# Kernel optimization log

Hardware: AMD Instinct MI355X
Metric: run time of the kernel (lower is better)

Reference implementation:

```python
import jax, jax.numpy as jnp
import numpy as np

DIM = 1024
H = 16
D = DIM // H
CS = 64  # chunk_size
SCALE = D ** -0.5


def setup_inputs() -> dict:
    key = jax.random.key(0)
    k1, k2, k3 = jax.random.split(key, 3)
    B, N = 4, 4096
    x = jax.random.normal(k1, (B, N, DIM), dtype=jnp.float32)
    # torch nn.Linear(dim, 3*dim, bias=False): y = x @ W.T, W:[3*dim, dim].
    # We store the transposed layout W_qkv:[dim, 3*dim] so y = x @ W_qkv.
    W_qkv = jax.random.normal(k2, (DIM, 3 * DIM), dtype=jnp.float32) * (DIM ** -0.5)
    W_out = jax.random.normal(k3, (DIM, DIM), dtype=jnp.float32) * (DIM ** -0.5)
    return {"x": x, "W_qkv": W_qkv, "W_out": W_out}


def reference(x, W_qkv, W_out):
    B, N, C = x.shape
    qkv = (x @ W_qkv).reshape(B, N, 3, H, D)
    qkv = jnp.transpose(qkv, (2, 0, 3, 1, 4))  # [3,B,H,N,D]
    q, k, v = qkv[0], qkv[1], qkv[2]
    # N chosen divisible by CS, so no padding needed (pad=0 branch).
    nc = N // CS
    q = q.reshape(B, H, nc, CS, D)
    k = k.reshape(B, H, nc, CS, D)
    v = v.reshape(B, H, nc, CS, D)
    # Local quadratic attention within each chunk, causal mask.
    attn = jnp.einsum('bhcqd,bhckd->bhcqk', q, k) * SCALE
    mask = jnp.triu(jnp.ones((CS, CS), dtype=bool), k=1)
    attn = jnp.where(mask, jnp.float32(-65000.0), attn)
    attn = jax.nn.softmax(attn, axis=-1)
    out_local = jnp.einsum('bhcqk,bhckd->bhcqd', attn, v)
    # Cross-chunk linear term (num_chunks > 1): mean-pooled K/V, exclusive cumsum.
    chunk_k = k.mean(axis=3)  # [B,H,nc,D]
    chunk_v = v.mean(axis=3)
    cum_k = jnp.cumsum(chunk_k, axis=2)
    cum_v = jnp.cumsum(chunk_v, axis=2)
    zeros = jnp.zeros((B, H, 1, D), dtype=x.dtype)
    cum_k = jnp.concatenate([zeros, cum_k[:, :, :-1]], axis=2)
    cum_v = jnp.concatenate([zeros, cum_v[:, :, :-1]], axis=2)
    cross = jax.nn.sigmoid(jnp.einsum('bhcsd,bhcd->bhcs', q, cum_k) * SCALE)
    out = out_local + cross[..., None] * cum_v[:, :, :, None, :] * 0.5
    out = out.reshape(B, H, N, D)
    out = jnp.transpose(out, (0, 2, 1, 3)).reshape(B, N, C)
    return out @ W_out
```

## Files before the change

### kernel.cpp

```cpp
#include <hip/hip_runtime.h>
#include <stdint.h>

typedef __attribute__((ext_vector_type(4))) float f32x4;
typedef __attribute__((ext_vector_type(8))) short short8;
typedef unsigned short u16;

#define NH 16
#define HD 64
#define SEQ 4096
#define BATCH 4
#define NROWS (BATCH * SEQ)
#define DIMC 1024
#define QKVC 3072
#define SCALE 0.125f

__device__ __forceinline__ u16 f2bf(float f) {
  union { float f; uint32_t u; } v; v.f = f;
  uint32_t u = v.u;
  uint32_t r = (u + 0x7fffu + ((u >> 16) & 1u)) >> 16;
  return (u16)r;
}
__device__ __forceinline__ float bf2f(u16 h) {
  union { uint32_t u; float f; } v; v.u = ((uint32_t)h) << 16;
  return v.f;
}

__global__ __launch_bounds__(256) void cvt_kernel(const float* __restrict__ in,
                                                  u16* __restrict__ out, int n4) {
  int i = blockIdx.x * 256 + threadIdx.x;
  if (i >= n4) return;
  float4 v = ((const float4*)in)[i];
  ushort4 o;
  o.x = f2bf(v.x); o.y = f2bf(v.y); o.z = f2bf(v.z); o.w = f2bf(v.w);
  ((ushort4*)out)[i] = o;
}

__global__ __launch_bounds__(256) void transpose_cvt(const float* __restrict__ in,
                                                     u16* __restrict__ out, int R, int C) {
  __shared__ float t[32][33];
  int nbx = C >> 5;
  int bx = blockIdx.x % nbx, by = blockIdx.x / nbx;
  int r0 = by << 5, c0 = bx << 5;
  int tid = threadIdx.x;
#pragma unroll
  for (int i = 0; i < 4; i++) {
    int id = i * 256 + tid; int lr = id >> 5, lc = id & 31;
    t[lr][lc] = in[(size_t)(r0 + lr) * C + (c0 + lc)];
  }
  __syncthreads();
#pragma unroll
  for (int i = 0; i < 4; i++) {
    int id = i * 256 + tid; int lr = id >> 5, lc = id & 31;
    out[(size_t)(c0 + lr) * R + (r0 + lc)] = f2bf(t[lc][lr]);
  }
}

template <int OUT_BF16, int DO_SUMS>
__global__ __launch_bounds__(512, 2) void gemm_bt(const u16* __restrict__ A,
                                                  const u16* __restrict__ Bt,
                                                  void* __restrict__ Cv,
                                                  float* __restrict__ chk,
                                                  float* __restrict__ chv,
                                                  int M, int N, int K) {
  __shared__ __align__(16) u16 lds2[2][32768];
  int nbx = N >> 8;
  int nwg = gridDim.x;
  int bid = blockIdx.x;
  int cpx = nwg >> 3;
  int swz = (bid & 7) * cpx + (bid >> 3);
  int bx = swz % nbx, by = swz / nbx;
  int tid = threadIdx.x, lane = tid & 63, wv = tid >> 6;
  int wr = wv >> 2, wc = wv & 3;
  int lr = lane & 15, g = lane >> 4;
  int rx = lr & 7;
  int rsub = lane >> 3;
  int clog = (lane & 7) ^ rsub;

  const u16* Ap = A + (size_t)(by * 256) * K;
  const u16* Bp = Bt + (size_t)(bx * 256) * K;

  f32x4 acc[8][4];
#pragma unroll
  for (int m = 0; m < 8; m++)
#pragma unroll
    for (int n = 0; n < 4; n++) acc[m][n] = (f32x4){0.f, 0.f, 0.f, 0.f};

  short8 a0[4][2], a1[4][2], b0[2][2], b1[2][2];

#define ISSUE_A(HALF, L, T) do {                                                \
    int ru_ = (HALF) * 128 + (L) * 64 + wv * 8;                                 \
    const u16* g_ = Ap + (size_t)(ru_ + rsub) * K + (T) * 64 + clog * 8;        \
    __builtin_amdgcn_global_load_lds(                                           \
        (const __attribute__((address_space(1))) uint32_t*)g_,                  \
        (__attribute__((address_space(3))) uint32_t*)&lds2[(T) & 1][ru_ * 64],  \
        16, 0, 0);                                                              \
  } while (0)

#define ISSUE_B(HALF, L, T) do {                                                \
    int ru_ = (HALF) * 128 + (L) * 64 + wv * 8;                                 \
    const u16* g_ = Bp + (size_t)(ru_ + rsub) * K + (T) * 64 + clog * 8;        \
    __builtin_amdgcn_global_load_lds(                                           \
        (const __attribute__((address_space(1))) uint32_t*)g_,                  \
        (__attribute__((address_space(3)))                                      \
             uint32_t*)&lds2[(T) & 1][16384 + ru_ * 64],                        \
        16, 0, 0);                                                              \
  } while (0)

#define LDA(DST, MH, T) do {                                                    \
    _Pragma("unroll")                                                           \
    for (int m2 = 0; m2 < 4; m2++) {                                            \
      int row_ = wr * 128 + ((MH) * 4 + m2) * 16 + lr;                          \
      const u16* bp_ = &lds2[(T) & 1][row_ * 64];                               \
      _Pragma("unroll")                                                         \
      for (int s = 0; s < 2; s++)                                               \
        DST[m2][s] = *(const short8*)(bp_ + (((s * 4 + g) ^ rx) << 3));         \
    }                                                                           \
  } while (0)

#define LDB(DST, NHh, T) do {                                                   \
    _Pragma("unroll")                                                           \
    for (int n2 = 0; n2 < 2; n2++) {                                            \
      int row_ = wc * 64 + ((NHh) * 2 + n2) * 16 + lr;                          \
      const u16* bp_ = &lds2[(T) & 1][16384 + row_ * 64];                       \
      _Pragma("unroll")                                                         \
      for (int s = 0; s < 2; s++)                                               \
        DST[n2][s] = *(const short8*)(bp_ + (((s * 4 + g) ^ rx) << 3));         \
    }                                                                           \
  } while (0)

#define MFMA_Q(MH, NHh, AA, BB) do {                                            \
    _Pragma("unroll")                                                           \
    for (int s = 0; s < 2; s++)                                                 \
      _Pragma("unroll")                                                         \
      for (int m2 = 0; m2 < 4; m2++)                                            \
        _Pragma("unroll")                                                       \
        for (int n2 = 0; n2 < 2; n2++)                                          \
          acc[(MH) * 4 + m2][(NHh) * 2 + n2] =                                  \
              __builtin_amdgcn_mfma_f32_16x16x32_bf16(                          \
                  AA[m2][s], BB[n2][s], acc[(MH) * 4 + m2][(NHh) * 2 + n2],     \
                  0, 0, 0);                                                     \
  } while (0)

  int NT = K >> 6;
  ISSUE_A(0, 0, 0); ISSUE_A(0, 1, 0); ISSUE_A(1, 0, 0); ISSUE_A(1, 1, 0);
  ISSUE_B(0, 0, 0); ISSUE_B(0, 1, 0); ISSUE_B(1, 0, 0); ISSUE_B(1, 1, 0);
  asm volatile("s_waitcnt vmcnt(0)" ::: "memory");
  __builtin_amdgcn_s_barrier();
  LDA(a0, 0, 0);
  LDB(b0, 0, 0);
  __builtin_amdgcn_sched_barrier(0);

  for (int t = 0; t < NT; t++) {
    LDB(b1, 1, t);
    if (t + 1 < NT) {
      ISSUE_A(0, 0, t + 1); ISSUE_A(0, 1, t + 1);
      ISSUE_A(1, 0, t + 1); ISSUE_A(1, 1, t + 1);
    }
    __builtin_amdgcn_sched_barrier(0);
    __builtin_amdgcn_s_setprio(1);
    MFMA_Q(0, 0, a0, b0);
    __builtin_amdgcn_s_setprio(0);
    __builtin_amdgcn_sched_barrier(0);
    __builtin_amdgcn_s_barrier();
    LDA(a1, 1, t);
    if (t + 1 < NT) {
      ISSUE_B(0, 0, t + 1); ISSUE_B(0, 1, t + 1);
      ISSUE_B(1, 0, t + 1); ISSUE_B(1, 1, t + 1);
    }
    __builtin_amdgcn_sched_barrier(0);
    __builtin_amdgcn_s_setprio(1);
    MFMA_Q(0, 1, a0, b1);
    __builtin_amdgcn_s_setprio(0);
    __builtin_amdgcn_sched_barrier(0);
    __builtin_amdgcn_s_barrier();
    __builtin_amdgcn_s_setprio(1);
    MFMA_Q(1, 0, a1, b0);
    __builtin_amdgcn_s_setprio(0);
    __builtin_amdgcn_sched_barrier(0);
    asm volatile("s_waitcnt vmcnt(0)" ::: "memory");
    __builtin_amdgcn_s_barrier();
    if (t + 1 < NT) {
      LDA(a0, 0, t + 1);
      LDB(b0, 0, t + 1);
    }
    __builtin_amdgcn_sched_barrier(0);
    __builtin_amdgcn_s_setprio(1);
    MFMA_Q(1, 1, a1, b1);
    __builtin_amdgcn_s_setprio(0);
    __builtin_amdgcn_sched_barrier(0);
    __builtin_amdgcn_s_barrier();
  }

#undef ISSUE_A
#undef ISSUE_B
#undef LDA
#undef LDB
#undef MFMA_Q

  int rb = by * 256 + wr * 128, cb = bx * 256 + wc * 64;

  if (DO_SUMS && cb >= 1024) {
#pragma unroll
    for (int mh = 0; mh < 2; mh++)
#pragma unroll
      for (int n = 0; n < 4; n++) {
        float sum = 0.f;
#pragma unroll
        for (int m = mh * 4; m < mh * 4 + 4; m++)
#pragma unroll
          for (int r = 0; r < 4; r++) sum += acc[m][n][r];
        sum += __shfl_xor(sum, 16);
        sum += __shfl_xor(sum, 32);
        if (g == 0) {
          int grb = rb + mh * 64;
          int b = grb >> 12, c = (grb >> 6) & 63;
          int cg = cb + n * 16 + lr;
          int col = cg & 1023;
          int h = col >> 6, d = col & 63;
          float* dst = (cg < 2048) ? chk : chv;
          dst[(((size_t)(b * 16 + h)) * 64 + c) * 64 + d] = sum * 0.015625f;
        }
      }
  }

#pragma unroll
  for (int m = 0; m < 8; m++)
#pragma unroll
    for (int n = 0; n < 4; n++)
#pragma unroll
      for (int r = 0; r < 4; r++) {
        int rg = rb + m * 16 + g * 4 + r;
        int cg = cb + n * 16 + lr;
        float v = acc[m][n][r];
        if (OUT_BF16)
          ((u16*)Cv)[(size_t)rg * N + cg] = f2bf(v);
        else
          ((float*)Cv)[(size_t)rg * N + cg] = v;
      }
}

__global__ void cumsum_excl(const float* __restrict__ ck, const float* __restrict__ cv,
                            float* __restrict__ cuk, float* __restrict__ cuv) {
  int bh = blockIdx.x;
  int d = threadIdx.x;
  float ak = 0.f, av = 0.f;
  for (int c = 0; c < 64; c++) {
    size_t i = ((size_t)bh * 64 + c) * 64 + d;
    cuk[i] = ak; cuv[i] = av;
    ak += ck[i]; av += cv[i];
  }
}

__global__ __launch_bounds__(256) void attn_kernel(const u16* __restrict__ qkv,
                                                   const float* __restrict__ cuk,
                                                   const float* __restrict__ cuv,
                                                   u16* __restrict__ out) {
  int blk = blockIdx.x;
  int c = blk & 63, h = (blk >> 6) & 15, b = blk >> 10;
  int row0 = b * SEQ + c * 64;
  __shared__ u16 q_s[64][80];
  __shared__ u16 k_s[64][80];
  __shared__ u16 vt_s[64][80];
  __shared__ u16 p_s[64][80];
  __shared__ u16 ck_s[64];
  __shared__ float cv_s[64];
  int tid = threadIdx.x;
  {
    int r = tid >> 2, qt = tid & 3;
    const u16* rp = qkv + (size_t)(row0 + r) * QKVC + h * 64 + qt * 16;
    uint4 q0 = *(const uint4*)rp;          uint4 q1 = *(const uint4*)(rp + 8);
    uint4 k0 = *(const uint4*)(rp + 1024); uint4 k1 = *(const uint4*)(rp + 1032);
    uint4 v0 = *(const uint4*)(rp + 2048); uint4 v1 = *(const uint4*)(rp + 2056);
    *(uint4*)&q_s[r][qt * 16] = q0;     *(uint4*)&q_s[r][qt * 16 + 8] = q1;
    *(uint4*)&k_s[r][qt * 16] = k0;     *(uint4*)&k_s[r][qt * 16 + 8] = k1;
    const u16* vv0 = (const u16*)&v0;   const u16* vv1 = (const u16*)&v1;
#pragma unroll
    for (int j = 0; j < 8; j++) vt_s[qt * 16 + j][r] = vv0[j];
#pragma unroll
    for (int j = 0; j < 8; j++) vt_s[qt * 16 + 8 + j][r] = vv1[j];
    if (tid < 64) {
      ck_s[tid] = f2bf(cuk[(size_t)blk * 64 + tid]);
      cv_s[tid] = cuv[(size_t)blk * 64 + tid];
    }
  }
  __syncthreads();

  int lane = tid & 63, w = tid >> 6;
  int lr = lane & 15, g = lane >> 4;
  f32x4 accS[4];
#pragma unroll
  for (int n = 0; n < 4; n++) accS[n] = (f32x4){0.f, 0.f, 0.f, 0.f};
  f32x4 accC = (f32x4){0.f, 0.f, 0.f, 0.f};
  short8 zf = (short8){0, 0, 0, 0, 0, 0, 0, 0};
#pragma unroll
  for (int kt = 0; kt < 2; kt++) {
    int lk = kt * 32 + g * 8;
    short8 af = *(const short8*)&q_s[w * 16 + lr][lk];
    short8 cf = (lr == 0) ? *(const short8*)&ck_s[lk] : zf;
    accC = __builtin_amdgcn_mfma_f32_16x16x32_bf16(af, cf, accC, 0, 0, 0);
#pragma unroll
    for (int n = 0; n < 4; n++) {
      short8 bf = *(const short8*)&k_s[n * 16 + lr][lk];
      accS[n] = __builtin_amdgcn_mfma_f32_16x16x32_bf16(af, bf, accS[n], 0, 0, 0);
    }
  }
  float crossv[4];
#pragma unroll
  for (int r4 = 0; r4 < 4; r4++) {
    int row = w * 16 + g * 4 + r4;
    float x[4];
    float mx = -3.4e38f;
#pragma unroll
    for (int n = 0; n < 4; n++) {
      int col = n * 16 + lr;
      x[n] = ((col & 63) > (row & 63)) ? -65000.0f : accS[n][r4] * SCALE;
      mx = fmaxf(mx, x[n]);
    }
    mx = fmaxf(mx, __shfl_xor(mx, 1));
    mx = fmaxf(mx, __shfl_xor(mx, 2));
    mx = fmaxf(mx, __shfl_xor(mx, 4));
    mx = fmaxf(mx, __shfl_xor(mx, 8));
    float p[4], sum = 0.f;
#pragma unroll
    for (int n = 0; n < 4; n++) { p[n] = __expf(x[n] - mx); sum += p[n]; }
    sum += __shfl_xor(sum, 1);
    sum += __shfl_xor(sum, 2);
    sum += __shfl_xor(sum, 4);
    sum += __shfl_xor(sum, 8);
    float inv = 1.0f / sum;
#pragma unroll
    for (int n = 0; n < 4; n++) p_s[row][n * 16 + lr] = f2bf(p[n] * inv);
    float sg = 1.0f / (1.0f + __expf(-accC[r4] * SCALE));
    crossv[r4] = __shfl(sg, (lane & 48));
  }
  __syncthreads();
  f32x4 accO[4];
#pragma unroll
  for (int n = 0; n < 4; n++) accO[n] = (f32x4){0.f, 0.f, 0.f, 0.f};
#pragma unroll
  for (int kt = 0; kt < 2; kt++) {
    int lk = kt * 32 + g * 8;
    short8 pf = *(const short8*)&p_s[w * 16 + lr][lk];
#pragma unroll
    for (int n = 0; n < 4; n++) {
      short8 vf = *(const short8*)&vt_s[n * 16 + lr][lk];
      accO[n] = __builtin_amdgcn_mfma_f32_16x16x32_bf16(pf, vf, accO[n], 0, 0, 0);
    }
  }
#pragma unroll
  for (int n = 0; n < 4; n++)
#pragma unroll
    for (int r4 = 0; r4 < 4; r4++) {
      int row = w * 16 + g * 4 + r4;
      int col = n * 16 + lr;
      float v = accO[n][r4] + crossv[r4] * cv_s[col] * 0.5f;
      out[(size_t)(row0 + row) * DIMC + h * 64 + col] = f2bf(v);
    }
}

extern "C" void kernel_launch(void* const* d_in, const int* in_sizes, int n_in,
                              void* d_out, int out_size, void* d_ws, size_t ws_size,
                              hipStream_t stream) {
  const float* x = (const float*)d_in[0];
  const float* Wqkv = (const float*)d_in[1];
  const float* Wout = (const float*)d_in[2];
  char* ws = (char*)d_ws;
  size_t off = 0;
  auto alloc = [&](size_t b) {
    void* p = ws + off;
    off += (b + 255) & ~(size_t)255;
    return p;
  };
  u16* xb = (u16*)alloc((size_t)NROWS * DIMC * 2);
  u16* wqt = (u16*)alloc((size_t)QKVC * DIMC * 2);
  u16* wot = (u16*)alloc((size_t)DIMC * DIMC * 2);
  u16* qkvb = (u16*)alloc((size_t)NROWS * QKVC * 2);
  float* chk = (float*)alloc((size_t)4096 * 64 * 4);
  float* chv = (float*)alloc((size_t)4096 * 64 * 4);
  float* cuk = (float*)alloc((size_t)4096 * 64 * 4);
  float* cuv = (float*)alloc((size_t)4096 * 64 * 4);
  u16* attnb = xb;

  cvt_kernel<<<16384, 256, 0, stream>>>(x, xb, NROWS * DIMC / 4);
  transpose_cvt<<<3072, 256, 0, stream>>>(Wqkv, wqt, DIMC, QKVC);
  transpose_cvt<<<1024, 256, 0, stream>>>(Wout, wot, DIMC, DIMC);
  gemm_bt<1, 1><<<768, 512, 0, stream>>>(xb, wqt, qkvb, chk, chv, NROWS, QKVC, DIMC);
  cumsum_excl<<<64, 64, 0, stream>>>(chk, chv, cuk, cuv);
  attn_kernel<<<4096, 256, 0, stream>>>(qkvb, cuk, cuv, attnb);
  gemm_bt<0, 0><<<256, 512, 0, stream>>>(attnb, wot, d_out, nullptr, nullptr,
                                         NROWS, DIMC, DIMC);
}
```

Before: 203.5 us.

## Deepen GEMM main loop pipeline with two-tile unroll and partial vmcnt waits

Restructures the GEMM K-loop into a two-iteration unrolled schedule that prefetches B two tiles ahead and A one tile ahead. Uses partial vmcnt/lgkmcnt waits instead of full drains, and reorders the quadrant MFMAs so LDS reads overlap with compute. The goal is to hide global-load latency behind MFMA work. It assumes NT is even, adds more barriers per tile, and depends on the exact in-flight load counts, so any mistake in those counts could cause races.

```diff
diff --git a/kernel.cpp b/kernel.cpp
--- a/kernel.cpp
+++ b/kernel.cpp
@@ -141,54 +141,80 @@
                   0, 0, 0);                                                     \
   } while (0)
 
+#define PH_PRE(NREADS)                                                          \
+    __builtin_amdgcn_sched_barrier(0);                                          \
+    if (NREADS >= 12) { asm volatile("s_waitcnt lgkmcnt(8)" ::: "memory"); }    \
+    __builtin_amdgcn_s_barrier();                                               \
+    asm volatile("s_waitcnt lgkmcnt(0)" ::: "memory");                          \
+    __builtin_amdgcn_sched_barrier(0);                                          \
+    __builtin_amdgcn_s_setprio(1)
+
+#define PH_POST                                                                 \
+    __builtin_amdgcn_s_setprio(0);                                              \
+    __builtin_amdgcn_sched_barrier(0);                                          \
+    __builtin_amdgcn_s_barrier()
+
   int NT = K >> 6;
   ISSUE_A(0, 0, 0); ISSUE_A(0, 1, 0); ISSUE_A(1, 0, 0); ISSUE_A(1, 1, 0);
   ISSUE_B(0, 0, 0); ISSUE_B(0, 1, 0); ISSUE_B(1, 0, 0); ISSUE_B(1, 1, 0);
-  asm volatile("s_waitcnt vmcnt(0)" ::: "memory");
+  ISSUE_B(0, 0, 1); ISSUE_B(0, 1, 1); ISSUE_B(1, 0, 1); ISSUE_B(1, 1, 1);
+  __builtin_amdgcn_sched_barrier(0);
+  asm volatile("s_waitcnt vmcnt(4)" ::: "memory");
+  __builtin_amdgcn_sched_barrier(0);
   __builtin_amdgcn_s_barrier();
-  LDA(a0, 0, 0);
-  LDB(b0, 0, 0);
-  __builtin_amdgcn_sched_barrier(0);
-
-  for (int t = 0; t < NT; t++) {
-    LDB(b1, 1, t);
-    if (t + 1 < NT) {
-      ISSUE_A(0, 0, t + 1); ISSUE_A(0, 1, t + 1);
-      ISSUE_A(1, 0, t + 1); ISSUE_A(1, 1, t + 1);
-    }
+
+  int NI = NT >> 1;
+  for (int i = 0; i < NI; i++) {
+    int T0 = 2 * i, T1 = 2 * i + 1;
+    int st0 = (T0 + 2 < NT), st1 = (T1 + 2 < NT);
+    LDA(a0, 0, T0); LDB(b0, 0, T0);
+    ISSUE_A(0, 0, T1); ISSUE_A(0, 1, T1);
+    PH_PRE(12);
+    MFMA_Q(0, 0, a0, b0);
+    PH_POST;
+    LDB(b1, 1, T0);
+    ISSUE_A(1, 0, T1); ISSUE_A(1, 1, T1);
+    PH_PRE(4);
+    MFMA_Q(0, 1, a0, b1);
+    PH_POST;
+    LDA(a1, 1, T0);
+    if (st0) { ISSUE_B(0, 0, T0 + 2); ISSUE_B(0, 1, T0 + 2); }
+    PH_PRE(8);
+    MFMA_Q(1, 1, a1, b1);
+    PH_POST;
+    if (st0) { ISSUE_B(1, 0, T0 + 2); ISSUE_B(1, 1, T0 + 2); }
     __builtin_amdgcn_sched_barrier(0);
-    __builtin_amdgcn_s_setprio(1);
-    MFMA_Q(0, 0, a0, b0);
-    __builtin_amdgcn_s_setprio(0);
-    __builtin_amdgcn_sched_barrier(0);
-    __builtin_amdgcn_s_barrier();
-    LDA(a1, 1, t);
-    if (t + 1 < NT) {
-      ISSUE_B(0, 0, t + 1); ISSUE_B(0, 1, t + 1);
-      ISSUE_B(1, 0, t + 1); ISSUE_B(1, 1, t + 1);
-    }
-    __builtin_amdgcn_sched_barrier(0);
-    __builtin_amdgcn_s_setprio(1);
-    MFMA_Q(0, 1, a0, b1);
-    __builtin_amdgcn_s_setprio(0);
+    if (st0) asm volatile("s_waitcnt vmcnt(4)" ::: "memory");
+    else     asm volatile("s_waitcnt vmcnt(0)" ::: "memory");
     __builtin_amdgcn_sched_barrier(0);
     __builtin_amdgcn_s_barrier();
     __builtin_amdgcn_s_setprio(1);
     MFMA_Q(1, 0, a1, b0);
-    __builtin_amdgcn_s_setprio(0);
+    PH_POST;
+    LDA(a0, 0, T1); LDB(b0, 0, T1);
+    if (st0) { ISSUE_A(0, 0, T0 + 2); ISSUE_A(0, 1, T0 + 2); }
+    PH_PRE(12);
+    MFMA_Q(0, 0, a0, b0);
+    PH_POST;
+    LDB(b1, 1, T1);
+    if (st0) { ISSUE_A(1, 0, T0 + 2); ISSUE_A(1, 1, T0 + 2); }
+    PH_PRE(4);
+    MFMA_Q(0, 1, a0, b1);
+    PH_POST;
+    LDA(a1, 1, T1);
+    if (st1) { ISSUE_B(0, 0, T1 + 2); ISSUE_B(0, 1, T1 + 2); }
+    PH_PRE(8);
+    MFMA_Q(1, 1, a1, b1);
+    PH_POST;
+    if (st1) { ISSUE_B(1, 0, T1 + 2); ISSUE_B(1, 1, T1 + 2); }
     __builtin_amdgcn_sched_barrier(0);
-    asm volatile("s_waitcnt vmcnt(0)" ::: "memory");
-    __builtin_amdgcn_s_barrier();
-    if (t + 1 < NT) {
-      LDA(a0, 0, t + 1);
-      LDB(b0, 0, t + 1);
-    }
-    __builtin_amdgcn_sched_barrier(0);
-    __builtin_amdgcn_s_setprio(1);
-    MFMA_Q(1, 1, a1, b1);
-    __builtin_amdgcn_s_setprio(0);
+    if (st1) asm volatile("s_waitcnt vmcnt(4)" ::: "memory");
+    else     asm volatile("s_waitcnt vmcnt(0)" ::: "memory");
     __builtin_amdgcn_sched_barrier(0);
     __builtin_amdgcn_s_barrier();
+    __builtin_amdgcn_s_setprio(1);
+    MFMA_Q(1, 0, a1, b0);
+    PH_POST;
   }
 
 #undef ISSUE_A
@@ -196,6 +222,8 @@
 #undef LDA
 #undef LDB
 #undef MFMA_Q
+#undef PH_PRE
+#undef PH_POST
 
   int rb = by * 256 + wr * 128, cb = bx * 256 + wc * 64;
 
```

Result: slower. 230.5 us (+13.2%).

## Switch GEMM to 32x32x16 MFMA with simplified double-buffered schedule; parallelize cumsum

Applied to the files above, without the earlier changes.

Rewrites the bf16 GEMM inner loop to use 32x32x16 MFMA tiles with 4x2 accumulators per wave. Each K-tile now reads all of its fragments up front and issues the next tile's loads into the other buffer, replacing the interleaved four-quadrant schedule with a single barrier per K step. Launch bounds drop to one block per CU, which frees registers but may lower occupancy. The exclusive cumsum now uses 256 threads per block, doing a two-level scan over four segments per head.

```diff
diff --git a/kernel.cpp b/kernel.cpp
--- a/kernel.cpp
+++ b/kernel.cpp
@@ -2,6 +2,7 @@
 #include <stdint.h>
 
 typedef __attribute__((ext_vector_type(4))) float f32x4;
+typedef __attribute__((ext_vector_type(16))) float f32x16;
 typedef __attribute__((ext_vector_type(8))) short short8;
 typedef unsigned short u16;
 
@@ -56,13 +57,13 @@
 }
 
 template <int OUT_BF16, int DO_SUMS>
-__global__ __launch_bounds__(512, 2) void gemm_bt(const u16* __restrict__ A,
+__global__ __launch_bounds__(512, 1) void gemm_bt(const u16* __restrict__ A,
                                                   const u16* __restrict__ Bt,
                                                   void* __restrict__ Cv,
                                                   float* __restrict__ chk,
                                                   float* __restrict__ chv,
                                                   int M, int N, int K) {
-  __shared__ __align__(16) u16 lds2[2][32768];
+  __shared__ __align__(16) u16 lds[65536];
   int nbx = N >> 8;
   int nwg = gridDim.x;
   int bid = blockIdx.x;
@@ -71,167 +72,148 @@
   int bx = swz % nbx, by = swz / nbx;
   int tid = threadIdx.x, lane = tid & 63, wv = tid >> 6;
   int wr = wv >> 2, wc = wv & 3;
-  int lr = lane & 15, g = lane >> 4;
-  int rx = lr & 7;
+  int l31 = lane & 31, hg = lane >> 5;
+  int rx = lane & 7;
   int rsub = lane >> 3;
   int clog = (lane & 7) ^ rsub;
 
   const u16* Ap = A + (size_t)(by * 256) * K;
   const u16* Bp = Bt + (size_t)(bx * 256) * K;
 
-  f32x4 acc[8][4];
-#pragma unroll
-  for (int m = 0; m < 8; m++)
-#pragma unroll
-    for (int n = 0; n < 4; n++) acc[m][n] = (f32x4){0.f, 0.f, 0.f, 0.f};
-
-  short8 a0[4][2], a1[4][2], b0[2][2], b1[2][2];
-
-#define ISSUE_A(HALF, L, T) do {                                                \
+  const u16* aB[4];
+  const u16* bB[4];
+#pragma unroll
+  for (int ks = 0; ks < 4; ks++) {
+    int ck = (((ks << 1) | hg) ^ rx) << 3;
+    aB[ks] = lds + (wr * 128 + l31) * 64 + ck;
+    bB[ks] = lds + 32768 + (wc * 64 + l31) * 64 + ck;
+  }
+
+  f32x16 acc[4][2];
+#pragma unroll
+  for (int m = 0; m < 4; m++)
+#pragma unroll
+    for (int n = 0; n < 2; n++)
+#pragma unroll
+      for (int r = 0; r < 16; r++) acc[m][n][r] = 0.f;
+
+  short8 af[4][4];
+  short8 bf[2][4];
+
+#define ISSUE_A(HALF, L, T, DBUF) do {                                          \
     int ru_ = (HALF) * 128 + (L) * 64 + wv * 8;                                 \
     const u16* g_ = Ap + (size_t)(ru_ + rsub) * K + (T) * 64 + clog * 8;        \
     __builtin_amdgcn_global_load_lds(                                           \
         (const __attribute__((address_space(1))) uint32_t*)g_,                  \
-        (__attribute__((address_space(3))) uint32_t*)&lds2[(T) & 1][ru_ * 64],  \
+        (__attribute__((address_space(3)))                                      \
+             uint32_t*)&lds[(DBUF) * 16384 + ru_ * 64],                         \
         16, 0, 0);                                                              \
   } while (0)
 
-#define ISSUE_B(HALF, L, T) do {                                                \
+#define ISSUE_B(HALF, L, T, DBUF) do {                                          \
     int ru_ = (HALF) * 128 + (L) * 64 + wv * 8;                                 \
     const u16* g_ = Bp + (size_t)(ru_ + rsub) * K + (T) * 64 + clog * 8;        \
     __builtin_amdgcn_global_load_lds(                                           \
         (const __attribute__((address_space(1))) uint32_t*)g_,                  \
         (__attribute__((address_space(3)))                                      \
-             uint32_t*)&lds2[(T) & 1][16384 + ru_ * 64],                        \
+             uint32_t*)&lds[32768 + (DBUF) * 16384 + ru_ * 64],                 \
         16, 0, 0);                                                              \
   } while (0)
 
-#define LDA(DST, MH, T) do {                                                    \
+#define LDA1(MT, KS, BUF) \
+    af[MT][KS] = *(const short8*)(aB[KS] + (BUF) * 16384 + (MT) * 2048)
+#define LDB1(NT, KS, BUF) \
+    bf[NT][KS] = *(const short8*)(bB[KS] + (BUF) * 16384 + (NT) * 2048)
+
+#define READ_KS(KS, BUF)                                                        \
+    LDA1(0, KS, BUF); LDA1(1, KS, BUF); LDA1(2, KS, BUF); LDA1(3, KS, BUF);     \
+    LDB1(0, KS, BUF); LDB1(1, KS, BUF)
+
+#define MFMA_KS(KS) do {                                                        \
     _Pragma("unroll")                                                           \
-    for (int m2 = 0; m2 < 4; m2++) {                                            \
-      int row_ = wr * 128 + ((MH) * 4 + m2) * 16 + lr;                          \
-      const u16* bp_ = &lds2[(T) & 1][row_ * 64];                               \
+    for (int mt = 0; mt < 4; mt++)                                              \
       _Pragma("unroll")                                                         \
-      for (int s = 0; s < 2; s++)                                               \
-        DST[m2][s] = *(const short8*)(bp_ + (((s * 4 + g) ^ rx) << 3));         \
-    }                                                                           \
+      for (int nt = 0; nt < 2; nt++)                                            \
+        acc[mt][nt] = __builtin_amdgcn_mfma_f32_32x32x16_bf16(                  \
+            af[mt][KS], bf[nt][KS], acc[mt][nt], 0, 0, 0);                      \
   } while (0)
 
-#define LDB(DST, NHh, T) do {                                                   \
-    _Pragma("unroll")                                                           \
-    for (int n2 = 0; n2 < 2; n2++) {                                            \
-      int row_ = wc * 64 + ((NHh) * 2 + n2) * 16 + lr;                          \
-      const u16* bp_ = &lds2[(T) & 1][16384 + row_ * 64];                       \
-      _Pragma("unroll")                                                         \
-      for (int s = 0; s < 2; s++)                                               \
-        DST[n2][s] = *(const short8*)(bp_ + (((s * 4 + g) ^ rx) << 3));         \
-    }                                                                           \
-  } while (0)
-
-#define MFMA_Q(MH, NHh, AA, BB) do {                                            \
-    _Pragma("unroll")                                                           \
-    for (int s = 0; s < 2; s++)                                                 \
-      _Pragma("unroll")                                                         \
-      for (int m2 = 0; m2 < 4; m2++)                                            \
-        _Pragma("unroll")                                                       \
-        for (int n2 = 0; n2 < 2; n2++)                                          \
-          acc[(MH) * 4 + m2][(NHh) * 2 + n2] =                                  \
-              __builtin_amdgcn_mfma_f32_16x16x32_bf16(                          \
-                  AA[m2][s], BB[n2][s], acc[(MH) * 4 + m2][(NHh) * 2 + n2],     \
-                  0, 0, 0);                                                     \
-  } while (0)
-
   int NT = K >> 6;
-  ISSUE_A(0, 0, 0); ISSUE_A(0, 1, 0); ISSUE_A(1, 0, 0); ISSUE_A(1, 1, 0);
-  ISSUE_B(0, 0, 0); ISSUE_B(0, 1, 0); ISSUE_B(1, 0, 0); ISSUE_B(1, 1, 0);
-  asm volatile("s_waitcnt vmcnt(0)" ::: "memory");
-  __builtin_amdgcn_s_barrier();
-  LDA(a0, 0, 0);
-  LDB(b0, 0, 0);
-  __builtin_amdgcn_sched_barrier(0);
+  ISSUE_A(0, 0, 0, 0); ISSUE_A(0, 1, 0, 0); ISSUE_A(1, 0, 0, 0); ISSUE_A(1, 1, 0, 0);
+  ISSUE_B(0, 0, 0, 0); ISSUE_B(0, 1, 0, 0); ISSUE_B(1, 0, 0, 0); ISSUE_B(1, 1, 0, 0);
+  __syncthreads();
 
   for (int t = 0; t < NT; t++) {
-    LDB(b1, 1, t);
+    int buf = t & 1;
+    READ_KS(0, buf);
+    READ_KS(1, buf);
+    __builtin_amdgcn_sched_barrier(0);
     if (t + 1 < NT) {
-      ISSUE_A(0, 0, t + 1); ISSUE_A(0, 1, t + 1);
-      ISSUE_A(1, 0, t + 1); ISSUE_A(1, 1, t + 1);
+      ISSUE_A(0, 0, t + 1, buf ^ 1); ISSUE_A(0, 1, t + 1, buf ^ 1);
+      ISSUE_A(1, 0, t + 1, buf ^ 1); ISSUE_A(1, 1, t + 1, buf ^ 1);
+    }
+    __builtin_amdgcn_sched_barrier(0);
+    READ_KS(2, buf);
+    READ_KS(3, buf);
+    __builtin_amdgcn_sched_barrier(0);
+    if (t + 1 < NT) {
+      ISSUE_B(0, 0, t + 1, buf ^ 1); ISSUE_B(0, 1, t + 1, buf ^ 1);
+      ISSUE_B(1, 0, t + 1, buf ^ 1); ISSUE_B(1, 1, t + 1, buf ^ 1);
     }
     __builtin_amdgcn_sched_barrier(0);
     __builtin_amdgcn_s_setprio(1);
-    MFMA_Q(0, 0, a0, b0);
+    MFMA_KS(0);
+    __builtin_amdgcn_sched_barrier(0);
+    MFMA_KS(1);
+    __builtin_amdgcn_sched_barrier(0);
+    MFMA_KS(2);
+    __builtin_amdgcn_sched_barrier(0);
+    MFMA_KS(3);
     __builtin_amdgcn_s_setprio(0);
-    __builtin_amdgcn_sched_barrier(0);
-    __builtin_amdgcn_s_barrier();
-    LDA(a1, 1, t);
-    if (t + 1 < NT) {
-      ISSUE_B(0, 0, t + 1); ISSUE_B(0, 1, t + 1);
-      ISSUE_B(1, 0, t + 1); ISSUE_B(1, 1, t + 1);
-    }
-    __builtin_amdgcn_sched_barrier(0);
-    __builtin_amdgcn_s_setprio(1);
-    MFMA_Q(0, 1, a0, b1);
-    __builtin_amdgcn_s_setprio(0);
-    __builtin_amdgcn_sched_barrier(0);
-    __builtin_amdgcn_s_barrier();
-    __builtin_amdgcn_s_setprio(1);
-    MFMA_Q(1, 0, a1, b0);
-    __builtin_amdgcn_s_setprio(0);
-    __builtin_amdgcn_sched_barrier(0);
-    asm volatile("s_waitcnt vmcnt(0)" ::: "memory");
-    __builtin_amdgcn_s_barrier();
-    if (t + 1 < NT) {
-      LDA(a0, 0, t + 1);
-      LDB(b0, 0, t + 1);
-    }
-    __builtin_amdgcn_sched_barrier(0);
-    __builtin_amdgcn_s_setprio(1);
-    MFMA_Q(1, 1, a1, b1);
-    __builtin_amdgcn_s_setprio(0);
-    __builtin_amdgcn_sched_barrier(0);
-    __builtin_amdgcn_s_barrier();
+    __syncthreads();
   }
 
 #undef ISSUE_A
 #undef ISSUE_B
-#undef LDA
-#undef LDB
-#undef MFMA_Q
+#undef LDA1
+#undef LDB1
+#undef READ_KS
+#undef MFMA_KS
 
   int rb = by * 256 + wr * 128, cb = bx * 256 + wc * 64;
 
   if (DO_SUMS && cb >= 1024) {
 #pragma unroll
-    for (int mh = 0; mh < 2; mh++)
-#pragma unroll
-      for (int n = 0; n < 4; n++) {
-        float sum = 0.f;
-#pragma unroll
-        for (int m = mh * 4; m < mh * 4 + 4; m++)
-#pragma unroll
-          for (int r = 0; r < 4; r++) sum += acc[m][n][r];
-        sum += __shfl_xor(sum, 16);
-        sum += __shfl_xor(sum, 32);
-        if (g == 0) {
-          int grb = rb + mh * 64;
+    for (int pair = 0; pair < 2; pair++)
+#pragma unroll
+      for (int nt = 0; nt < 2; nt++) {
+        float s = 0.f;
+#pragma unroll
+        for (int mi = 0; mi < 2; mi++)
+#pragma unroll
+          for (int r = 0; r < 16; r++) s += acc[pair * 2 + mi][nt][r];
+        s += __shfl_xor(s, 32);
+        if (hg == 0) {
+          int grb = rb + pair * 64;
           int b = grb >> 12, c = (grb >> 6) & 63;
-          int cg = cb + n * 16 + lr;
+          int cg = cb + nt * 32 + l31;
           int col = cg & 1023;
           int h = col >> 6, d = col & 63;
           float* dst = (cg < 2048) ? chk : chv;
-          dst[(((size_t)(b * 16 + h)) * 64 + c) * 64 + d] = sum * 0.015625f;
+          dst[(((size_t)(b * 16 + h)) * 64 + c) * 64 + d] = s * 0.015625f;
         }
       }
   }
 
 #pragma unroll
-  for (int m = 0; m < 8; m++)
-#pragma unroll
-    for (int n = 0; n < 4; n++)
-#pragma unroll
-      for (int r = 0; r < 4; r++) {
-        int rg = rb + m * 16 + g * 4 + r;
-        int cg = cb + n * 16 + lr;
-        float v = acc[m][n][r];
+  for (int mt = 0; mt < 4; mt++)
+#pragma unroll
+    for (int nt = 0; nt < 2; nt++)
+#pragma unroll
+      for (int r = 0; r < 16; r++) {
+        int rg = rb + mt * 32 + (r & 3) + 8 * (r >> 2) + 4 * hg;
+        int cg = cb + nt * 32 + l31;
+        float v = acc[mt][nt][r];
         if (OUT_BF16)
           ((u16*)Cv)[(size_t)rg * N + cg] = f2bf(v);
         else
@@ -239,13 +221,25 @@
       }
 }
 
-__global__ void cumsum_excl(const float* __restrict__ ck, const float* __restrict__ cv,
-                            float* __restrict__ cuk, float* __restrict__ cuv) {
+__global__ __launch_bounds__(256) void cumsum_excl(const float* __restrict__ ck,
+                                                   const float* __restrict__ cv,
+                                                   float* __restrict__ cuk,
+                                                   float* __restrict__ cuv) {
+  __shared__ float qk[4][64], qv[4][64];
   int bh = blockIdx.x;
-  int d = threadIdx.x;
+  int d = threadIdx.x & 63, q = threadIdx.x >> 6;
+  size_t base = ((size_t)bh * 64) * 64 + d;
+  float sk = 0.f, sv = 0.f;
+  for (int c = q * 16; c < q * 16 + 16; c++) {
+    sk += ck[base + (size_t)c * 64];
+    sv += cv[base + (size_t)c * 64];
+  }
+  qk[q][d] = sk; qv[q][d] = sv;
+  __syncthreads();
   float ak = 0.f, av = 0.f;
-  for (int c = 0; c < 64; c++) {
-    size_t i = ((size_t)bh * 64 + c) * 64 + d;
+  for (int p = 0; p < q; p++) { ak += qk[p][d]; av += qv[p][d]; }
+  for (int c = q * 16; c < q * 16 + 16; c++) {
+    size_t i = base + (size_t)c * 64;
     cuk[i] = ak; cuv[i] = av;
     ak += ck[i]; av += cv[i];
   }
@@ -385,7 +379,7 @@
   transpose_cvt<<<3072, 256, 0, stream>>>(Wqkv, wqt, DIMC, QKVC);
   transpose_cvt<<<1024, 256, 0, stream>>>(Wout, wot, DIMC, DIMC);
   gemm_bt<1, 1><<<768, 512, 0, stream>>>(xb, wqt, qkvb, chk, chv, NROWS, QKVC, DIMC);
-  cumsum_excl<<<64, 64, 0, stream>>>(chk, chv, cuk, cuv);
+  cumsum_excl<<<64, 256, 0, stream>>>(chk, chv, cuk, cuv);
   attn_kernel<<<4096, 256, 0, stream>>>(qkvb, cuk, cuv, attnb);
   gemm_bt<0, 0><<<256, 512, 0, stream>>>(attnb, wot, d_out, nullptr, nullptr,
                                          NROWS, DIMC, DIMC);
```

Measured after the change: 222.5 us. +9.3%, slower.
